# Optimization experiments

Measured on AMD Instinct MI355X. Metric: run time of the kernel, lower is better.

The kernel has to match this reference:

```python
import jax, jax.numpy as jnp
import numpy as np

B, H, W, C = 16, 32, 32, 256
N = H * W


def setup_inputs() -> dict:
    key = jax.random.key(0)
    ks = jax.random.split(key, 8)
    x = jax.random.normal(ks[0], (B, H, W, C), dtype=jnp.float32)
    # nn.LazyLinear(C): weight (C, C), bias (C,)
    scale = 1.0 / np.sqrt(C)
    Wq = jax.random.uniform(ks[1], (C, C), jnp.float32, -scale, scale)
    bq = jax.random.uniform(ks[2], (C,), jnp.float32, -scale, scale)
    Wk = jax.random.uniform(ks[3], (C, C), jnp.float32, -scale, scale)
    bk = jax.random.uniform(ks[4], (C,), jnp.float32, -scale, scale)
    Wv = jax.random.uniform(ks[5], (C, C), jnp.float32, -scale, scale)
    bv = jax.random.uniform(ks[6], (C,), jnp.float32, -scale, scale)
    # torch.randn(H, H*W, W)
    Wp = jax.random.normal(ks[7], (H, N, W), dtype=jnp.float32)
    return {"x": x, "Wq": Wq, "bq": bq, "Wk": Wk, "bk": bk,
            "Wv": Wv, "bv": bv, "Wp": Wp}


def reference(x, Wq, bq, Wk, bk, Wv, bv, Wp):
    b, h, w, c = x.shape
    n = h * w
    # Linear projections (torch Linear: x @ W^T + b), flatten spatial dims to N tokens
    q = (jnp.einsum('bhwc,dc->bhwd', x, Wq) + bq).reshape(b, n, c)
    k = (jnp.einsum('bhwc,dc->bhwd', x, Wk) + bk).reshape(b, n, c)
    v = (jnp.einsum('bhwc,dc->bhwd', x, Wv) + bv).reshape(b, n, c)
    # Unscaled attention over the N spatial tokens (no 1/sqrt(C) in the original)
    scores = jnp.einsum('bnc,bmc->bnm', q, k)          # (B, N, N)
    attn = jax.nn.softmax(scores, axis=-1)
    qkv = jnp.einsum('bnm,bmc->bnc', attn, v)           # (B, N, C)
    # z = (qkv^T [B,1,C,N] @ Wp [H,N,W]).transpose(-2,-1) -> (B, H, W, C)
    z = jnp.einsum('bnc,hnw->bhwc', qkv, Wp)
    return z
```

## Files before the change

### kernel.cpp

```cpp
#include <hip/hip_runtime.h>
#include <hip/hip_bf16.h>

#define BB 16
#define NN 1024
#define CC 256

typedef __attribute__((ext_vector_type(8))) short bf16x8;
typedef __attribute__((ext_vector_type(4))) float f32x4;

#define GPTR(p) ((const __attribute__((address_space(1))) void*)(p))
#define LPTR(p) ((__attribute__((address_space(3))) void*)(p))

__device__ __forceinline__ unsigned short f2bf(float f) {
  union { float f; unsigned u; } v; v.f = f;
  unsigned r = v.u + 0x7FFFu + ((v.u >> 16) & 1u);
  return (unsigned short)(r >> 16);
}

#define NCAST 17155
__global__ __launch_bounds__(256) void preprocess(
    const float* __restrict__ x,
    const float* __restrict__ Wq, const float* __restrict__ Wk,
    const float* __restrict__ Wv,
    const float* __restrict__ bq, const float* __restrict__ bk,
    const float* __restrict__ bv,
    const float* __restrict__ Wp,
    unsigned short* __restrict__ xb,
    unsigned short* __restrict__ wqkvb,
    float* __restrict__ bqkv,
    unsigned short* __restrict__ Amat) {
  __shared__ float tile[32][33];
  int blk = blockIdx.x;
  if (blk < NCAST) {
    const int NX = BB * NN * CC;
    const int NW = CC * CC;
    int i = blk * 256 + threadIdx.x;
    if (i < NX) { xb[i] = f2bf(x[i]); return; }
    int j = i - NX;
    if (j < 3 * NW) {
      const float* w = (j < NW) ? Wq : (j < 2 * NW ? Wk : Wv);
      wqkvb[j] = f2bf(w[j % NW]);
      return;
    }
    int jj = j - 3 * NW;
    if (jj < 3 * CC) {
      const float* bb = (jj < CC) ? bq : (jj < 2 * CC ? bk : bv);
      bqkv[jj] = bb[jj % CC];
    }
    return;
  }
  int wb = blk - NCAST;
  int h = wb >> 5;
  int n0 = (wb & 31) * 32;
#pragma unroll
  for (int j = 0; j < 4; j++) {
    int idx = threadIdx.x + j * 256;
    int a = idx >> 5, wc = idx & 31;
    tile[a][wc] = Wp[(size_t)h * (NN * 32) + (size_t)(n0 + a) * 32 + wc];
  }
  __syncthreads();
#pragma unroll
  for (int j = 0; j < 4; j++) {
    int idx = threadIdx.x + j * 256;
    int wc = idx >> 5, a = idx & 31;
    Amat[(size_t)(h * 32 + wc) * NN + n0 + a] = f2bf(tile[a][wc]);
  }
}

template <int BIAS_MODE, int F32OUT>
__global__ __launch_bounds__(256) void gemm_tile(
    const unsigned short* __restrict__ A, int lda, long sA,
    const unsigned short* __restrict__ Bt, int ldb, long sB,
    const float* __restrict__ bias,
    void* __restrict__ Out, int ldo, long sO, int K) {
  __shared__ unsigned short As[2 * 128 * 32];
  __shared__ unsigned short Bs[2 * 64 * 32];
  int b = blockIdx.x;
  int m0 = blockIdx.y * 128;
  int n0 = blockIdx.z * 64;
  int t = threadIdx.x;
  int w = t >> 6, lane = t & 63;
  int wm = (w >> 1) * 64, wn = (w & 1) * 32;
  int r = lane & 15, g = lane >> 4;

  const unsigned short* Ab = A + (long)b * sA;
  const unsigned short* Bb = Bt + (long)b * sB;

  int srow = t >> 2;
  int scol = (t & 3) * 8;

  f32x4 acc[4][2];
#pragma unroll
  for (int i = 0; i < 4; i++)
#pragma unroll
    for (int j = 0; j < 2; j++) acc[i][j] = (f32x4){0.f, 0.f, 0.f, 0.f};

  for (int k0 = 0; k0 < K; k0 += 64) {
    __syncthreads();
#pragma unroll
    for (int kh = 0; kh < 2; kh++) {
#pragma unroll
      for (int jj = 0; jj < 2; jj++) {
        __builtin_amdgcn_global_load_lds(
            GPTR(Ab + (long)(m0 + srow + jj * 64) * lda + k0 + kh * 32 + scol),
            LPTR(&As[kh * 4096 + jj * 2048 + t * 8]), 16, 0, 0);
      }
      __builtin_amdgcn_global_load_lds(
          GPTR(Bb + (long)(n0 + srow) * ldb + k0 + kh * 32 + scol),
          LPTR(&Bs[kh * 2048 + t * 8]), 16, 0, 0);
    }
    __syncthreads();
#pragma unroll
    for (int kh = 0; kh < 2; kh++) {
      bf16x8 af[4], bfr[2];
#pragma unroll
      for (int ti = 0; ti < 4; ti++)
        af[ti] = *(const bf16x8*)&As[kh * 4096 + (wm + ti * 16 + r) * 32 + g * 8];
#pragma unroll
      for (int tj = 0; tj < 2; tj++)
        bfr[tj] = *(const bf16x8*)&Bs[kh * 2048 + (wn + tj * 16 + r) * 32 + g * 8];
#pragma unroll
      for (int ti = 0; ti < 4; ti++)
#pragma unroll
        for (int tj = 0; tj < 2; tj++)
          acc[ti][tj] = __builtin_amdgcn_mfma_f32_16x16x32_bf16(af[ti], bfr[tj], acc[ti][tj], 0, 0, 0);
    }
  }

#pragma unroll
  for (int ti = 0; ti < 4; ti++) {
#pragma unroll
    for (int tj = 0; tj < 2; tj++) {
      int col = n0 + wn + tj * 16 + r;
      float bc = (BIAS_MODE == 1) ? bias[col] : 0.0f;
#pragma unroll
      for (int rr = 0; rr < 4; rr++) {
        int row = m0 + wm + ti * 16 + g * 4 + rr;
        float val = acc[ti][tj][rr] + bc;
        long oidx = (long)b * sO + (long)row * ldo + col;
        if (F32OUT)
          ((float*)Out)[oidx] = val;
        else
          ((unsigned short*)Out)[oidx] = f2bf(val);
      }
    }
  }
}

__global__ __launch_bounds__(256) void gemm_qkv(
    const unsigned short* __restrict__ A,
    const unsigned short* __restrict__ Bt,
    const float* __restrict__ bias,
    unsigned short* __restrict__ Qb, unsigned short* __restrict__ Kb,
    unsigned short* __restrict__ Vtb) {
  __shared__ unsigned short As[2 * 128 * 32];
  __shared__ unsigned short Bs[2 * 128 * 32];
  int b = blockIdx.x;
  int m0 = blockIdx.y * 128;
  int n0 = blockIdx.z * 128;
  int t = threadIdx.x;
  int w = t >> 6, lane = t & 63;
  int wm = (w >> 1) * 64, wn = (w & 1) * 64;
  int r = lane & 15, g = lane >> 4;

  const unsigned short* Ab = A + (long)b * NN * CC;
  int srow = t >> 2;
  int scol = (t & 3) * 8;

  f32x4 acc[4][4];
#pragma unroll
  for (int i = 0; i < 4; i++)
#pragma unroll
    for (int j = 0; j < 4; j++) acc[i][j] = (f32x4){0.f, 0.f, 0.f, 0.f};

  for (int k0 = 0; k0 < CC; k0 += 64) {
    __syncthreads();
#pragma unroll
    for (int kh = 0; kh < 2; kh++) {
#pragma unroll
      for (int jj = 0; jj < 2; jj++) {
        __builtin_amdgcn_global_load_lds(
            GPTR(Ab + (long)(m0 + srow + jj * 64) * CC + k0 + kh * 32 + scol),
            LPTR(&As[kh * 4096 + jj * 2048 + t * 8]), 16, 0, 0);
        __builtin_amdgcn_global_load_lds(
            GPTR(Bt + (long)(n0 + srow + jj * 64) * CC + k0 + kh * 32 + scol),
            LPTR(&Bs[kh * 4096 + jj * 2048 + t * 8]), 16, 0, 0);
      }
    }
    __syncthreads();
#pragma unroll
    for (int kh = 0; kh < 2; kh++) {
      bf16x8 af[4], bfr[4];
#pragma unroll
      for (int ti = 0; ti < 4; ti++)
        af[ti] = *(const bf16x8*)&As[kh * 4096 + (wm + ti * 16 + r) * 32 + g * 8];
#pragma unroll
      for (int tj = 0; tj < 4; tj++)
        bfr[tj] = *(const bf16x8*)&Bs[kh * 4096 + (wn + tj * 16 + r) * 32 + g * 8];
#pragma unroll
      for (int ti = 0; ti < 4; ti++)
#pragma unroll
        for (int tj = 0; tj < 4; tj++)
          acc[ti][tj] = __builtin_amdgcn_mfma_f32_16x16x32_bf16(af[ti], bfr[tj], acc[ti][tj], 0, 0, 0);
    }
  }

  int seg = n0 >> 8;
#pragma unroll
  for (int ti = 0; ti < 4; ti++) {
#pragma unroll
    for (int tj = 0; tj < 4; tj++) {
      int col = n0 + wn + tj * 16 + r;
      int c = col & 255;
      float bc = bias[col];
#pragma unroll
      for (int rr = 0; rr < 4; rr++) {
        int row = m0 + wm + ti * 16 + g * 4 + rr;
        float val = acc[ti][tj][rr] + bc;
        long base = (long)b * NN * CC;
        if (seg == 0) {
          Qb[base + (long)row * CC + c] = f2bf(val);
        } else if (seg == 1) {
          Kb[base + ((long)(c >> 5) * NN + row) * 32 + (c & 31)] = f2bf(val);
        } else {
          Vtb[base + ((((long)(c >> 4) * 128 + (row >> 3)) * 16 + (c & 15)) * 8 + (row & 7))] = f2bf(val);
        }
      }
    }
  }
}

__global__ __launch_bounds__(512, 4) void attn_fused(
    const unsigned short* __restrict__ Q,
    const unsigned short* __restrict__ Kt,
    const unsigned short* __restrict__ Vt,
    unsigned short* __restrict__ QKVt) {
  __shared__ unsigned short ShBuf[32 * 1024];
  __shared__ float red[4][2][16];
  int b = blockIdx.x;
  int n0 = blockIdx.y * 32;
  int t = threadIdx.x;
  int w = t >> 6, lane = t & 63;
  int rg = w >> 2, ch = w & 3;
  int r = lane & 15, g = lane >> 4;

  const unsigned short* kslab = Kt + (long)b * NN * CC;
#pragma unroll
  for (int j = 0; j < 8; j++) {
    __builtin_amdgcn_global_load_lds(
        GPTR(kslab + j * 4096 + t * 8),
        LPTR(&ShBuf[j * 4096 + t * 8]), 16, 0, 0);
  }
  const unsigned short* qbase = Q + ((long)b * NN + n0 + rg * 16 + r) * CC + g * 8;
  bf16x8 qv = *(const bf16x8*)qbase;

  f32x4 acc[16];
#pragma unroll
  for (int tt = 0; tt < 16; tt++) acc[tt] = (f32x4){0.f, 0.f, 0.f, 0.f};

  for (int kk = 0; kk < 8; kk++) {
    __syncthreads();
    bf16x8 qnext;
    if (kk < 7) qnext = *(const bf16x8*)(qbase + (kk + 1) * 32);
#pragma unroll
    for (int tt = 0; tt < 16; tt++) {
      bf16x8 bv = *(const bf16x8*)&ShBuf[(ch * 256 + tt * 16 + r) * 32 + g * 8];
      acc[tt] = __builtin_amdgcn_mfma_f32_16x16x32_bf16(qv, bv, acc[tt], 0, 0, 0);
    }
    if (kk < 7) {
      __syncthreads();
#pragma unroll
      for (int j = 0; j < 8; j++) {
        __builtin_amdgcn_global_load_lds(
            GPTR(kslab + (long)(kk + 1) * NN * 32 + j * 4096 + t * 8),
            LPTR(&ShBuf[j * 4096 + t * 8]), 16, 0, 0);
      }
      qv = qnext;
    }
  }

  float mrow[4];
#pragma unroll
  for (int rr = 0; rr < 4; rr++) {
    float m = acc[0][rr];
#pragma unroll
    for (int tt = 1; tt < 16; tt++) m = fmaxf(m, acc[tt][rr]);
#pragma unroll
    for (int d = 1; d < 16; d <<= 1) m = fmaxf(m, __shfl_xor(m, d, 64));
    mrow[rr] = m;
  }
  if (r == 0) {
#pragma unroll
    for (int rr = 0; rr < 4; rr++) red[ch][rg][g * 4 + rr] = mrow[rr];
  }
  __syncthreads();
#pragma unroll
  for (int rr = 0; rr < 4; rr++) {
    float m = red[0][rg][g * 4 + rr];
#pragma unroll
    for (int c2 = 1; c2 < 4; c2++) m = fmaxf(m, red[c2][rg][g * 4 + rr]);
    mrow[rr] = m;
  }
  __syncthreads();
  float ssum[4];
#pragma unroll
  for (int rr = 0; rr < 4; rr++) {
    float s = 0.f;
#pragma unroll
    for (int tt = 0; tt < 16; tt++) {
      float e = exp2f((acc[tt][rr] - mrow[rr]) * 1.44269504088896f);
      acc[tt][rr] = e;
      s += e;
    }
#pragma unroll
    for (int d = 1; d < 16; d <<= 1) s += __shfl_xor(s, d, 64);
    ssum[rr] = s;
  }
  if (r == 0) {
#pragma unroll
    for (int rr = 0; rr < 4; rr++) red[ch][rg][g * 4 + rr] = ssum[rr];
  }
  __syncthreads();
#pragma unroll
  for (int rr = 0; rr < 4; rr++) {
    float s = red[0][rg][g * 4 + rr] + red[1][rg][g * 4 + rr] +
              red[2][rg][g * 4 + rr] + red[3][rg][g * 4 + rr];
    float inv = 1.0f / s;
    int prow = rg * 16 + g * 4 + rr;
    int sw = prow & 7;
#pragma unroll
    for (int tt = 0; tt < 16; tt++) {
      int col = ch * 256 + tt * 16 + r;
      int chunk = (col >> 3) ^ sw;
      ShBuf[prow * 1024 + chunk * 8 + (col & 7)] = f2bf(acc[tt][rr] * inv);
    }
  }
  __syncthreads();

  const unsigned short* vbase = Vt + (long)b * NN * CC;
  int cw = w * 32;
  f32x4 o[2][2];
#pragma unroll
  for (int i = 0; i < 2; i++)
#pragma unroll
    for (int j = 0; j < 2; j++) o[i][j] = (f32x4){0.f, 0.f, 0.f, 0.f};

#pragma unroll 4
  for (int m0 = 0; m0 < NN; m0 += 32) {
    bf16x8 ar[2], br[2];
#pragma unroll
    for (int bt = 0; bt < 2; bt++) {
      long vidx = (((long)((cw >> 4) + bt) * 128 + (m0 >> 3) + g) * 16 + r) * 8;
      br[bt] = *(const bf16x8*)(vbase + vidx);
    }
#pragma unroll
    for (int rt = 0; rt < 2; rt++) {
      int prow = rt * 16 + r;
      int chunk = ((m0 >> 3) + g) ^ (prow & 7);
      ar[rt] = *(const bf16x8*)&ShBuf[prow * 1024 + chunk * 8];
    }
#pragma unroll
    for (int rt = 0; rt < 2; rt++)
#pragma unroll
      for (int bt = 0; bt < 2; bt++)
        o[rt][bt] = __builtin_amdgcn_mfma_f32_16x16x32_bf16(ar[rt], br[bt], o[rt][bt], 0, 0, 0);
  }

  unsigned short* obase = QKVt + (long)b * NN * CC;
#pragma unroll
  for (int rt = 0; rt < 2; rt++) {
#pragma unroll
    for (int bt = 0; bt < 2; bt++) {
      int c = cw + bt * 16 + r;
#pragma unroll
      for (int rr = 0; rr < 4; rr++) {
        int n = n0 + rt * 16 + g * 4 + rr;
        obase[(long)c * NN + n] = f2bf(o[rt][bt][rr]);
      }
    }
  }
}

extern "C" void kernel_launch(void* const* d_in, const int* in_sizes, int n_in,
                              void* d_out, int out_size, void* d_ws, size_t ws_size,
                              hipStream_t stream) {
  const float* x  = (const float*)d_in[0];
  const float* Wq = (const float*)d_in[1];
  const float* bq = (const float*)d_in[2];
  const float* Wk = (const float*)d_in[3];
  const float* bk = (const float*)d_in[4];
  const float* Wv = (const float*)d_in[5];
  const float* bv = (const float*)d_in[6];
  const float* Wp = (const float*)d_in[7];
  float* out = (float*)d_out;

  const long BNC = (long)BB * NN * CC;

  char* p = (char*)d_ws;
  unsigned short* xb    = (unsigned short*)p; p += BNC * 2;
  unsigned short* wqkvb = (unsigned short*)p; p += 3L * CC * CC * 2;
  float*          bqkv  = (float*)p;          p += 4096;
  unsigned short* Amat  = (unsigned short*)p; p += (long)NN * NN * 2;
  unsigned short* Qb    = (unsigned short*)p; p += BNC * 2;
  unsigned short* Ktb   = (unsigned short*)p; p += BNC * 2;
  unsigned short* Vtb   = (unsigned short*)p; p += BNC * 2;
  unsigned short* QKVt  = (unsigned short*)p; p += BNC * 2;

  preprocess<<<NCAST + 1024, 256, 0, stream>>>(
      x, Wq, Wk, Wv, bq, bk, bv, Wp, xb, wqkvb, bqkv, Amat);

  gemm_qkv<<<dim3(BB, 8, 6), 256, 0, stream>>>(xb, wqkvb, bqkv, Qb, Ktb, Vtb);

  attn_fused<<<dim3(BB, NN / 32), 512, 0, stream>>>(Qb, Ktb, Vtb, QKVt);

  gemm_tile<0, 1><<<dim3(BB, 8, 4), 256, 0, stream>>>(
      Amat, NN, 0L, QKVt, NN, (long)NN * CC, nullptr,
      out, CC, (long)NN * CC, NN);
}
```

Before: 151.2 us.

## Load K fragments directly from global per wave, dropping LDS staging in QK^T

```diff
diff --git a/kernel.cpp b/kernel.cpp
--- a/kernel.cpp
+++ b/kernel.cpp
@@ -236,103 +236,113 @@
     const unsigned short* __restrict__ Vt,
     unsigned short* __restrict__ QKVt) {
   __shared__ unsigned short ShBuf[32 * 1024];
-  __shared__ float red[4][2][16];
+  __shared__ float red[8][32];
   int b = blockIdx.x;
   int n0 = blockIdx.y * 32;
   int t = threadIdx.x;
   int w = t >> 6, lane = t & 63;
-  int rg = w >> 2, ch = w & 3;
   int r = lane & 15, g = lane >> 4;
 
-  const unsigned short* kslab = Kt + (long)b * NN * CC;
-#pragma unroll
-  for (int j = 0; j < 8; j++) {
-    __builtin_amdgcn_global_load_lds(
-        GPTR(kslab + j * 4096 + t * 8),
-        LPTR(&ShBuf[j * 4096 + t * 8]), 16, 0, 0);
-  }
-  const unsigned short* qbase = Q + ((long)b * NN + n0 + rg * 16 + r) * CC + g * 8;
-  bf16x8 qv = *(const bf16x8*)qbase;
-
-  f32x4 acc[16];
-#pragma unroll
-  for (int tt = 0; tt < 16; tt++) acc[tt] = (f32x4){0.f, 0.f, 0.f, 0.f};
-
+  const unsigned short* kbase =
+      Kt + (long)b * NN * CC + ((long)(w * 128 + r)) * 32 + g * 8;
+  const unsigned short* qbase =
+      Q + ((long)b * NN + n0 + r) * CC + g * 8;
+
+  f32x4 acc[2][8];
+#pragma unroll
+  for (int i = 0; i < 2; i++)
+#pragma unroll
+    for (int j = 0; j < 8; j++) acc[i][j] = (f32x4){0.f, 0.f, 0.f, 0.f};
+
+#pragma unroll
   for (int kk = 0; kk < 8; kk++) {
-    __syncthreads();
-    bf16x8 qnext;
-    if (kk < 7) qnext = *(const bf16x8*)(qbase + (kk + 1) * 32);
-#pragma unroll
-    for (int tt = 0; tt < 16; tt++) {
-      bf16x8 bv = *(const bf16x8*)&ShBuf[(ch * 256 + tt * 16 + r) * 32 + g * 8];
-      acc[tt] = __builtin_amdgcn_mfma_f32_16x16x32_bf16(qv, bv, acc[tt], 0, 0, 0);
-    }
-    if (kk < 7) {
-      __syncthreads();
-#pragma unroll
-      for (int j = 0; j < 8; j++) {
-        __builtin_amdgcn_global_load_lds(
-            GPTR(kslab + (long)(kk + 1) * NN * 32 + j * 4096 + t * 8),
-            LPTR(&ShBuf[j * 4096 + t * 8]), 16, 0, 0);
-      }
-      qv = qnext;
-    }
-  }
-
-  float mrow[4];
-#pragma unroll
-  for (int rr = 0; rr < 4; rr++) {
-    float m = acc[0][rr];
-#pragma unroll
-    for (int tt = 1; tt < 16; tt++) m = fmaxf(m, acc[tt][rr]);
-#pragma unroll
-    for (int d = 1; d < 16; d <<= 1) m = fmaxf(m, __shfl_xor(m, d, 64));
-    mrow[rr] = m;
+    bf16x8 qa0 = *(const bf16x8*)(qbase + kk * 32);
+    bf16x8 qa1 = *(const bf16x8*)(qbase + 16 * CC + kk * 32);
+    bf16x8 kf[8];
+#pragma unroll
+    for (int ct = 0; ct < 8; ct++)
+      kf[ct] = *(const bf16x8*)(kbase + (long)kk * (NN * 32) + ct * 512);
+#pragma unroll
+    for (int ct = 0; ct < 8; ct++) {
+      acc[0][ct] = __builtin_amdgcn_mfma_f32_16x16x32_bf16(qa0, kf[ct], acc[0][ct], 0, 0, 0);
+      acc[1][ct] = __builtin_amdgcn_mfma_f32_16x16x32_bf16(qa1, kf[ct], acc[1][ct], 0, 0, 0);
+    }
+  }
+
+  float mrow[2][4];
+#pragma unroll
+  for (int rt = 0; rt < 2; rt++) {
+#pragma unroll
+    for (int rr = 0; rr < 4; rr++) {
+      float m = acc[rt][0][rr];
+#pragma unroll
+      for (int ct = 1; ct < 8; ct++) m = fmaxf(m, acc[rt][ct][rr]);
+#pragma unroll
+      for (int d = 1; d < 16; d <<= 1) m = fmaxf(m, __shfl_xor(m, d, 64));
+      mrow[rt][rr] = m;
+    }
   }
   if (r == 0) {
 #pragma unroll
-    for (int rr = 0; rr < 4; rr++) red[ch][rg][g * 4 + rr] = mrow[rr];
+    for (int rt = 0; rt < 2; rt++)
+#pragma unroll
+      for (int rr = 0; rr < 4; rr++)
+        red[w][rt * 16 + g * 4 + rr] = mrow[rt][rr];
   }
   __syncthreads();
 #pragma unroll
-  for (int rr = 0; rr < 4; rr++) {
-    float m = red[0][rg][g * 4 + rr];
-#pragma unroll
-    for (int c2 = 1; c2 < 4; c2++) m = fmaxf(m, red[c2][rg][g * 4 + rr]);
-    mrow[rr] = m;
+  for (int rt = 0; rt < 2; rt++) {
+#pragma unroll
+    for (int rr = 0; rr < 4; rr++) {
+      int row = rt * 16 + g * 4 + rr;
+      float m = red[0][row];
+#pragma unroll
+      for (int w2 = 1; w2 < 8; w2++) m = fmaxf(m, red[w2][row]);
+      mrow[rt][rr] = m;
+    }
   }
   __syncthreads();
-  float ssum[4];
-#pragma unroll
-  for (int rr = 0; rr < 4; rr++) {
-    float s = 0.f;
-#pragma unroll
-    for (int tt = 0; tt < 16; tt++) {
-      float e = exp2f((acc[tt][rr] - mrow[rr]) * 1.44269504088896f);
-      acc[tt][rr] = e;
-      s += e;
-    }
-#pragma unroll
-    for (int d = 1; d < 16; d <<= 1) s += __shfl_xor(s, d, 64);
-    ssum[rr] = s;
+  float ssum[2][4];
+#pragma unroll
+  for (int rt = 0; rt < 2; rt++) {
+#pragma unroll
+    for (int rr = 0; rr < 4; rr++) {
+      float s = 0.f;
+#pragma unroll
+      for (int ct = 0; ct < 8; ct++) {
+        float e = exp2f((acc[rt][ct][rr] - mrow[rt][rr]) * 1.44269504088896f);
+        acc[rt][ct][rr] = e;
+        s += e;
+      }
+#pragma unroll
+      for (int d = 1; d < 16; d <<= 1) s += __shfl_xor(s, d, 64);
+      ssum[rt][rr] = s;
+    }
   }
   if (r == 0) {
 #pragma unroll
-    for (int rr = 0; rr < 4; rr++) red[ch][rg][g * 4 + rr] = ssum[rr];
+    for (int rt = 0; rt < 2; rt++)
+#pragma unroll
+      for (int rr = 0; rr < 4; rr++)
+        red[w][rt * 16 + g * 4 + rr] = ssum[rt][rr];
   }
   __syncthreads();
 #pragma unroll
-  for (int rr = 0; rr < 4; rr++) {
-    float s = red[0][rg][g * 4 + rr] + red[1][rg][g * 4 + rr] +
-              red[2][rg][g * 4 + rr] + red[3][rg][g * 4 + rr];
-    float inv = 1.0f / s;
-    int prow = rg * 16 + g * 4 + rr;
-    int sw = prow & 7;
-#pragma unroll
-    for (int tt = 0; tt < 16; tt++) {
-      int col = ch * 256 + tt * 16 + r;
-      int chunk = (col >> 3) ^ sw;
-      ShBuf[prow * 1024 + chunk * 8 + (col & 7)] = f2bf(acc[tt][rr] * inv);
+  for (int rt = 0; rt < 2; rt++) {
+#pragma unroll
+    for (int rr = 0; rr < 4; rr++) {
+      int row = rt * 16 + g * 4 + rr;
+      float s = 0.f;
+#pragma unroll
+      for (int w2 = 0; w2 < 8; w2++) s += red[w2][row];
+      float inv = 1.0f / s;
+      int sw = row & 7;
+#pragma unroll
+      for (int ct = 0; ct < 8; ct++) {
+        int col = w * 128 + ct * 16 + r;
+        int chunk = (col >> 3) ^ sw;
+        ShBuf[row * 1024 + chunk * 8 + (col & 7)] = f2bf(acc[rt][ct][rr] * inv);
+      }
     }
   }
   __syncthreads();
```

Measured after the change: 168.0 us. 1.11x slower.
